# Performance work log

Hardware: AMD Instinct MI355X
Metric: run time of the kernel (lower is better)

## Reference

```python
import jax, jax.numpy as jnp
import numpy as np

K = 20
EPS = 1e-5
N = 4096


def lrelu(x):
    return jnp.where(x >= 0, x, 0.2 * x)


def bn(x, g, b, m, v):
    # eval-mode BatchNorm over channel dim 1
    shape = [1] * x.ndim
    shape[1] = -1
    inv = g / jnp.sqrt(v + EPS)
    return (x - m.reshape(shape)) * inv.reshape(shape) + b.reshape(shape)


def get_graph_feature(x):
    # Faithful to repo: num_points = x.shape[1], remaining dims fold into channels.
    p = x.shape[1]
    x2d = x.reshape(-1, p)              # (C, P)
    xx = jnp.sum(x2d * x2d, axis=0)     # (P,)
    dist = 2.0 * (x2d.T @ x2d) - xx[:, None] - xx[None, :]  # -||xi-xj||^2, (P, P)
    idx = jax.lax.top_k(dist, K)[1]     # (P, K) nearest neighbors (incl. self)
    xt = x2d.T                          # (P, C)
    feat = xt[idx]                      # (P, K, C) neighbor gather
    ctr = jnp.broadcast_to(xt[:, None, :], feat.shape)
    out = jnp.concatenate([feat - ctr, ctr], axis=-1)  # (P, K, 2C)
    return out.transpose(2, 0, 1)[None]                # (1, 2C, P, K)


def setup_inputs():
    key = jax.random.key(0)
    ks = jax.random.split(key, 16)

    def w(k_, o, c):
        return jax.random.normal(k_, (o, c), jnp.float32) / float(np.sqrt(c))

    def bnp(k_, c):
        k1, k2, k3, k4 = jax.random.split(k_, 4)
        return (1.0 + 0.1 * jax.random.normal(k1, (c,), jnp.float32),
                0.1 * jax.random.normal(k2, (c,), jnp.float32),
                0.1 * jax.random.normal(k3, (c,), jnp.float32),
                jax.random.uniform(k4, (c,), jnp.float32, minval=0.5, maxval=1.5))

    g1, b1, m1, v1 = bnp(ks[1], 64)
    g2, b2, m2, v2 = bnp(ks[2], 64)
    g3, b3, m3, v3 = bnp(ks[3], 128)
    g4, b4, m4, v4 = bnp(ks[4], 256)
    g5, b5, m5, v5 = bnp(ks[5], 512)
    return dict(
        x=jax.random.normal(ks[0], (3, N), jnp.float32),
        w1=w(ks[6], 64, 6), g1=g1, b1=b1, m1=m1, v1=v1,
        w2=w(ks[7], 64, 64), g2=g2, b2=b2, m2=m2, v2=v2,
        w3=w(ks[8], 128, 64), g3=g3, b3=b3, m3=m3, v3=v3,
        w4=w(ks[9], 256, 128), g4=g4, b4=b4, m4=m4, v4=v4,
        w5=w(ks[10], 512, 256), g5=g5, b5=b5, m5=m5, v5=v5,
        lw1=w(ks[11], 512, 1024),
        lw2=w(ks[12], 256, 512),
        lb2=0.1 * jax.random.normal(ks[13], (256,), jnp.float32),
        ow=w(ks[14], 11, 256),
        ob=0.1 * jax.random.normal(ks[15], (11,), jnp.float32),
    )


def reference(x, w1, g1, b1, m1, v1, w2, g2, b2, m2, v2, w3, g3, b3, m3, v3,
              w4, g4, b4, m4, v4, w5, g5, b5, m5, v5, lw1, lw2, lb2, ow, ob):
    conv2d = lambda w_, f_: jnp.einsum('oc,bcpk->bopk', w_, f_)

    f = get_graph_feature(x)                                   # (1, 6, N, K)
    h = lrelu(bn(conv2d(w1, f), g1, b1, m1, v1))
    x1 = jnp.max(h, axis=-1)                                   # (1, 64, N)

    f = jnp.swapaxes(get_graph_feature(x1), 1, 2)              # (1, 64, 2N, K)
    h = lrelu(bn(conv2d(w2, f), g2, b2, m2, v2))
    x2 = jnp.max(h, axis=-1)                                   # (1, 64, 2N)

    f = jnp.swapaxes(get_graph_feature(x2), 1, 2)              # (1, 64, 4N, K)
    h = lrelu(bn(conv2d(w3, f), g3, b3, m3, v3))
    x3 = jnp.max(h, axis=-1)                                   # (1, 128, 4N)

    f = jnp.swapaxes(get_graph_feature(x3), 1, 2)              # (1, 128, 8N, K)
    h = lrelu(bn(conv2d(w4, f), g4, b4, m4, v4))
    x4 = jnp.max(h, axis=-1)                                   # (1, 256, 8N)

    h5 = lrelu(bn(jnp.einsum('oc,bcp->bop', w5, x4), g5, b5, m5, v5))  # (1, 512, 8N)
    pmax = jnp.max(h5, axis=-1)
    pavg = jnp.mean(h5, axis=-1)
    z = jnp.concatenate([pmax, pavg], axis=1)                  # (1, 1024)
    z = lrelu(z @ lw1.T)                                       # (1, 512); dropout = eval identity
    z = lrelu(z @ lw2.T + lb2)                                 # (1, 256)
    logits = z @ ow.T + ob                                     # (1, 11)
    return jax.nn.softmax(logits, axis=1)
```

## Files before the change

kernel.cpp:

```cpp
#include <hip/hip_runtime.h>
#include <hip/hip_bf16.h>
#include <float.h>
#include <math.h>

#define DEV __device__ __forceinline__

DEV float lrelu(float x) { return x >= 0.f ? x : 0.2f * x; }

constexpr int N = 4096, KNN = 20;

typedef __attribute__((ext_vector_type(4))) float f32x4;
typedef __attribute__((ext_vector_type(8))) short s16x8;

constexpr size_t OFF_SC1 = 0,    OFF_SH1 = 64;
constexpr size_t OFF_SC2 = 128,  OFF_SH2 = 192;
constexpr size_t OFF_SC3 = 256,  OFF_SH3 = 384;
constexpr size_t OFF_SC4 = 512,  OFF_SH4 = 768;
constexpr size_t OFF_SC5 = 1024, OFF_SH5 = 1536;
constexpr size_t OFF_X1 = 2048;
constexpr size_t OFF_X2 = OFF_X1 + (size_t)64*4096;
constexpr size_t OFF_X3 = OFF_X2 + (size_t)64*8192;
constexpr size_t OFF_X4 = OFF_X3 + (size_t)128*16384;
constexpr size_t OFF_A  = OFF_X4 + (size_t)256*32768;
constexpr size_t OFF_GP = OFF_A + (size_t)256*21*128;
constexpr size_t OFF_PM = OFF_GP + (size_t)64*128*128;
constexpr size_t OFF_PS = OFF_PM + (size_t)512*256;
constexpr size_t OFF_Z0 = OFF_PS + (size_t)512*256;
constexpr size_t OFF_Z1 = OFF_Z0 + 1024;
constexpr size_t OFF_Z2 = OFF_Z1 + 512;
constexpr size_t OFF_IDX = OFF_Z2 + 256;
constexpr size_t WS_NEEDED_BYTES = OFF_IDX * 4 + (size_t)N * KNN * 4;
constexpr size_t OFF_ABF = OFF_A;
constexpr size_t OFF_W5BF = OFF_A + 524288;

__global__ void k_ws_sentinel(float* out, float mb) {
  int t = threadIdx.x;
  if (t < 11) out[t] = 1.0e6f + mb;
}

__global__ __launch_bounds__(512) void k_bn_pre(
    const float* g1, const float* b1, const float* m1, const float* v1,
    const float* g2, const float* b2, const float* m2, const float* v2,
    const float* g3, const float* b3, const float* m3, const float* v3,
    const float* g4, const float* b4, const float* m4, const float* v4,
    const float* g5, const float* b5, const float* m5, const float* v5,
    float* ws) {
  int t = threadIdx.x;
  const float* G[5] = {g1,g2,g3,g4,g5};
  const float* B[5] = {b1,b2,b3,b4,b5};
  const float* M[5] = {m1,m2,m3,m4,m5};
  const float* V[5] = {v1,v2,v3,v4,v5};
  const size_t SC[5] = {OFF_SC1,OFF_SC2,OFF_SC3,OFF_SC4,OFF_SC5};
  const size_t SH[5] = {OFF_SH1,OFF_SH2,OFF_SH3,OFF_SH4,OFF_SH5};
  const int CN[5] = {64,64,128,256,512};
  for (int s = 0; s < 5; ++s) {
    for (int i = t; i < CN[s]; i += 512) {
      float scale = G[s][i] / sqrtf(V[s][i] + 1e-5f);
      ws[SC[s] + i] = scale;
      ws[SH[s] + i] = B[s][i] - M[s][i] * scale;
    }
  }
}

__global__ __launch_bounds__(256) void k_s1_topk(const float* x, int* idx) {
  __shared__ float d[N];
  __shared__ float vsh[256];
  __shared__ int ish[256];
  int i = blockIdx.x, t = threadIdx.x;
  {
    #pragma clang fp contract(off)
    float xi0 = x[i], xi1 = x[N + i], xi2 = x[2*N + i];
    float sqi = xi0*xi0 + xi1*xi1 + xi2*xi2;
    for (int j = t; j < N; j += 256) {
      float xj0 = x[j], xj1 = x[N+j], xj2 = x[2*N+j];
      float sqj = xj0*xj0 + xj1*xj1 + xj2*xj2;
      float p = xi0*xj0 + xi1*xj1 + xi2*xj2;
      d[j] = (2.f*p - sqi) - sqj;
    }
  }
  __syncthreads();
  for (int k = 0; k < KNN; ++k) {
    float bv = -FLT_MAX; int bi = N;
    for (int j = t; j < N; j += 256) { float v = d[j]; if (v > bv) { bv = v; bi = j; } }
    vsh[t] = bv; ish[t] = bi;
    __syncthreads();
    for (int s = 128; s > 0; s >>= 1) {
      if (t < s) {
        float v2 = vsh[t+s]; int i2 = ish[t+s];
        if (v2 > vsh[t] || (v2 == vsh[t] && i2 < ish[t])) { vsh[t] = v2; ish[t] = i2; }
      }
      __syncthreads();
    }
    if (t == 0) { idx[i*KNN + k] = ish[0]; d[ish[0]] = -FLT_MAX; }
    __syncthreads();
  }
}

__global__ __launch_bounds__(256) void k_s1_conv(const float* x, const float* w1g,
                                                 const int* idx, const float* sc, const float* sh, float* x1) {
  __shared__ int idxs[64][KNN];
  __shared__ float xs[3][64];
  __shared__ float wsh[4][6];
  int t = threadIdx.x, bx = blockIdx.x, by = blockIdx.y;
  int i0 = bx * 64;
  for (int u = t; u < 64*KNN; u += 256) idxs[u/KNN][u%KNN] = idx[(size_t)(i0 + u/KNN)*KNN + u%KNN];
  for (int u = t; u < 3*64; u += 256) xs[u/64][u%64] = x[(size_t)(u/64)*N + i0 + (u%64)];
  for (int u = t; u < 24; u += 256) wsh[u/6][u%6] = w1g[(size_t)(by*4 + u/6)*6 + u%6];
  __syncthreads();
  int il = t & 63, ol = t >> 6;
  int o = by*4 + ol, i = i0 + il;
  float xi0 = xs[0][il], xi1 = xs[1][il], xi2 = xs[2][il];
  float w0 = wsh[ol][0], w1v = wsh[ol][1], w2v = wsh[ol][2];
  float w3v = wsh[ol][3], w4v = wsh[ol][4], w5v = wsh[ol][5];
  float ctr = w3v*xi0 + w4v*xi1 + w5v*xi2;
  float scale = sc[o], shift = sh[o];
  float best = -FLT_MAX;
  for (int k = 0; k < KNN; ++k) {
    int j = idxs[il][k];
    float h = w0*(x[j] - xi0) + w1v*(x[N+j] - xi1) + w2v*(x[2*N+j] - xi2) + ctr;
    h = lrelu(h*scale + shift);
    best = fmaxf(best, h);
  }
  x1[(size_t)o*N + i] = best;
}

template<int P>
__global__ __launch_bounds__(256) void k_gram_partial(const float* prev, int C, float* gp) {
  constexpr int BI = P / 16;
  __shared__ float ysh[32][P];
  int b = blockIdx.x, t = threadIdx.x;
  int R = C / 64;
  int base = b * R;
  float acc[BI][BI] = {};
  int i0 = (t >> 4) * BI, j0 = (t & 15) * BI;
  for (int r0 = 0; r0 < R; r0 += 32) {
    for (int u = t; u < 32*P; u += 256) ysh[u/P][u%P] = prev[(size_t)(base + r0 + u/P)*P + (u%P)];
    __syncthreads();
    for (int r = 0; r < 32; ++r) {
      float yi[BI], yj[BI];
      #pragma unroll
      for (int a = 0; a < BI; ++a) { yi[a] = ysh[r][i0+a]; yj[a] = ysh[r][j0+a]; }
      #pragma unroll
      for (int a = 0; a < BI; ++a)
        #pragma unroll
        for (int c = 0; c < BI; ++c) acc[a][c] += yi[a]*yj[c];
    }
    __syncthreads();
  }
  for (int a = 0; a < BI; ++a)
    for (int c = 0; c < BI; ++c)
      gp[(size_t)b*P*P + (size_t)(i0+a)*P + (j0+c)] = acc[a][c];
}

template<int P>
__global__ __launch_bounds__(128) void k_dist_topk(const float* gp, int* idx) {
  __shared__ float dsh[P];
  __shared__ float diag[P];
  __shared__ float vsh[128];
  __shared__ int ish[128];
  int i = blockIdx.x, t = threadIdx.x;
  if (t < P) {
    float gij = 0.f, gjj = 0.f;
    for (int b = 0; b < 64; ++b) {
      gij += gp[(size_t)b*P*P + (size_t)i*P + t];
      gjj += gp[(size_t)b*P*P + (size_t)t*P + t];
    }
    diag[t] = gjj;
    dsh[t] = gij;
  }
  __syncthreads();
  if (t < P) dsh[t] = (2.f*dsh[t] - diag[i]) - diag[t];
  __syncthreads();
  for (int k = 0; k < KNN; ++k) {
    float bv = -FLT_MAX; int bi = P;
    if (t < P) { bv = dsh[t]; bi = t; }
    vsh[t] = bv; ish[t] = bi;
    __syncthreads();
    for (int s = 64; s > 0; s >>= 1) {
      if (t < s) {
        float v2 = vsh[t+s]; int i2 = ish[t+s];
        if (v2 > vsh[t] || (v2 == vsh[t] && i2 < ish[t])) { vsh[t] = v2; ish[t] = i2; }
      }
      __syncthreads();
    }
    if (t == 0) { idx[i*KNN + k] = ish[0]; dsh[ish[0]] = -FLT_MAX; }
    __syncthreads();
  }
}

template<int P>
__global__ __launch_bounds__(64) void k_build_A(const float* w, const int* idx, int O, float* A) {
  __shared__ float row[64][P];
  int t = threadIdx.x;
  int r = blockIdx.x*64 + t;
  if (r < O*21) {
    int o = r / 21, kk = r % 21;
    float* my = row[t];
    if (kk == 20) {
      for (int i2 = 0; i2 < P; ++i2) my[i2] = w[(size_t)o*P + i2];
    } else {
      for (int i2 = 0; i2 < P; ++i2) my[i2] = 0.f;
      for (int j = 0; j < P; ++j) my[idx[j*KNN + kk]] += w[(size_t)o*P + j];
    }
    for (int i2 = 0; i2 < P; ++i2) A[(size_t)r*P + i2] = my[i2];
  }
}

__global__ __launch_bounds__(64) void k_build_A_bf(const float* w, const int* idx, __hip_bfloat16* A) {
  __shared__ float row[64][128];
  int t = threadIdx.x;
  int r = blockIdx.x*64 + t;
  int o = r >> 5, kk = r & 31;
  float* my = row[t];
  if (kk == 20) {
    for (int i2 = 0; i2 < 128; ++i2) my[i2] = w[(size_t)o*128 + i2];
  } else if (kk < 20) {
    for (int i2 = 0; i2 < 128; ++i2) my[i2] = 0.f;
    for (int j = 0; j < 128; ++j) my[idx[j*KNN + kk]] += w[(size_t)o*128 + j];
  } else {
    for (int i2 = 0; i2 < 128; ++i2) my[i2] = 0.f;
  }
  for (int i2 = 0; i2 < 128; ++i2) A[(size_t)r*128 + i2] = __float2bfloat16(my[i2]);
}

__global__ __launch_bounds__(256) void k_f32_to_bf16(const float* in, __hip_bfloat16* out) {
  size_t base = ((size_t)blockIdx.x*256 + threadIdx.x) * 16;
  #pragma unroll
  for (int j = 0; j < 4; ++j) {
    float4 v = *(const float4*)(in + base + j*4);
    __hip_bfloat16 tmp[4] = {__float2bfloat16(v.x), __float2bfloat16(v.y),
                             __float2bfloat16(v.z), __float2bfloat16(v.w)};
    *(ushort4*)(out + base + j*4) = *(const ushort4*)tmp;
  }
}

__global__ __launch_bounds__(256) void k_conv4_mfma(const __hip_bfloat16* Abf, const __hip_bfloat16* Xbf,
                                                    const float* sc, const float* sh, float* x4) {
  constexpr int RA = 64, MT = 256;
  __shared__ char As[RA*256];
  __shared__ char Bs[MT*256];
  int t = threadIdx.x, bx = blockIdx.x, by = blockIdx.y;
  int m0 = bx*MT, rbase = by*RA;
  for (int u = t; u < RA*16; u += 256) {
    int row = u >> 4, k8 = u & 15;
    s16x8 v = *(const s16x8*)(Abf + ((size_t)(rbase+row) << 7) + (k8 << 3));
    *(s16x8*)(As + (row << 8) + ((k8 << 4) ^ ((row & 7) << 4))) = v;
  }
  for (int u = t; u < MT*16; u += 256) {
    int row = u >> 4, k8 = u & 15;
    s16x8 v = *(const s16x8*)(Xbf + ((size_t)(m0+row) << 7) + (k8 << 3));
    *(s16x8*)(Bs + (row << 8) + ((k8 << 4) ^ ((row & 7) << 4))) = v;
  }
  __syncthreads();
  int lane = t & 63, w = t >> 6;
  int col = lane & 15, lg = lane >> 4;
  f32x4 acc[4][4] = {};
  #pragma unroll
  for (int ks = 0; ks < 4; ++ks) {
    int kbyte = ks*64 + lg*16;
    s16x8 a[4], b[4];
    #pragma unroll
    for (int at = 0; at < 4; ++at) { int r = at*16 + col; a[at] = *(const s16x8*)(As + (r<<8) + (kbyte ^ ((r&7)<<4))); }
    #pragma unroll
    for (int bt = 0; bt < 4; ++bt) { int r = w*64 + bt*16 + col; b[bt] = *(const s16x8*)(Bs + (r<<8) + (kbyte ^ ((r&7)<<4))); }
    #pragma unroll
    for (int at = 0; at < 4; ++at)
      #pragma unroll
      for (int bt = 0; bt < 4; ++bt)
        acc[at][bt] = __builtin_amdgcn_mfma_f32_16x16x32_bf16(a[at], b[bt], acc[at][bt], 0, 0, 0);
  }
  int o0 = by*2;
  #pragma unroll
  for (int ol = 0; ol < 2; ++ol) {
    float scale = sc[o0+ol], shift = sh[o0+ol];
    #pragma unroll
    for (int bt = 0; bt < 4; ++bt) {
      float h2b = __shfl(acc[2*ol+1][bt][0], 16 + col);
      float mx = -FLT_MAX;
      #pragma unroll
      for (int q = 0; q < 4; ++q) {
        mx = fmaxf(mx, lrelu((acc[2*ol][bt][q] - h2b)*scale + shift));
        float v1 = lrelu((acc[2*ol+1][bt][q] - h2b)*scale + shift);
        if (lg == 0) mx = fmaxf(mx, v1);
      }
      mx = fmaxf(mx, __shfl_xor(mx, 16));
      mx = fmaxf(mx, __shfl_xor(mx, 32));
      float ctr = lrelu(h2b*scale + shift);
      if ((lg >> 1) == ol) {
        float val = (lg & 1) ? ctr : mx;
        size_t p = (size_t)m0 + w*64 + bt*16 + col + ((lg & 1) ? 16384 : 0);
        x4[(size_t)(o0+ol)*32768 + p] = val;
      }
    }
  }
}

template<int P>
__global__ __launch_bounds__(256) void k_fused_conv(const float* prev, const float* A,
                                                    const float* sc, const float* sh,
                                                    int C, float* outx) {
  constexpr int TO = 8, ROWS = TO*21;
  __shared__ float Ash[ROWS][65];
  __shared__ float Bsh[64][132];
  int bx = blockIdx.x, by = blockIdx.y, t = threadIdx.x;
  int m0 = bx*128;
  int rowbase = by*ROWS;
  int ol = t >> 5, mg = t & 31;
  float acc[21][4] = {};
  for (int ic = 0; ic < P/64; ++ic) {
    for (int u = t; u < ROWS*64; u += 256) {
      int rr = u >> 6, cc = u & 63;
      Ash[rr][cc] = A[(size_t)(rowbase + rr)*P + ic*64 + cc];
    }
    for (int u = t; u < 64*128; u += 256) {
      int mr = u >> 6, ii = u & 63;
      Bsh[ii][mr] = prev[(size_t)(m0 + mr)*P + ic*64 + ii];
    }
    __syncthreads();
    for (int i = 0; i < 64; ++i) {
      float v0 = Bsh[i][mg*4+0], v1 = Bsh[i][mg*4+1], v2 = Bsh[i][mg*4+2], v3 = Bsh[i][mg*4+3];
      #pragma unroll
      for (int kk = 0; kk < 21; ++kk) {
        float a = Ash[ol*21 + kk][i];
        acc[kk][0] += a*v0; acc[kk][1] += a*v1; acc[kk][2] += a*v2; acc[kk][3] += a*v3;
      }
    }
    __syncthreads();
  }
  int o = by*TO + ol;
  float scale = sc[o], shift = sh[o];
  size_t C2 = 2*(size_t)C;
  #pragma unroll
  for (int mm = 0; mm < 4; ++mm) {
    int m = m0 + mg*4 + mm;
    float h2 = acc[20][mm];
    float ctr = lrelu(h2*scale + shift);
    float best = -FLT_MAX;
    #pragma unroll
    for (int kk = 0; kk < 20; ++kk) {
      float v = lrelu((acc[kk][mm] - h2)*scale + shift);
      best = fmaxf(best, v);
    }
    outx[(size_t)o*C2 + m] = best;
    outx[(size_t)o*C2 + C + m] = ctr;
  }
}

__global__ __launch_bounds__(256) void k_s5_mfma(const float* x4, const __hip_bfloat16* w5bf,
                                                 const float* sc, const float* sh,
                                                 float* pm, float* ps) {
  __shared__ char smem[8192 + 32768];
  __shared__ float redm[64][4];
  __shared__ float reds[64][4];
  int t = threadIdx.x, bx = blockIdx.x, by = blockIdx.y;
  int p0 = bx*256, o0 = by*64;
  int lane = t & 63, w = t >> 6;
  int lrow = lane & 15, lg = lane >> 4;
  char* As = smem;
  char* Bs = smem + 8192;
  f32x4 acc[4][4] = {};
  for (int c0 = 0; c0 < 256; c0 += 64) {
    for (int u = t; u < 64*8; u += 256) {
      int row = u >> 3, k8 = u & 7;
      s16x8 v = *(const s16x8*)(w5bf + (size_t)(o0+row)*256 + c0 + k8*8);
      *(s16x8*)(As + row*128 + ((k8*16) ^ ((row&7)<<4))) = v;
    }
    #pragma unroll
    for (int i = 0; i < 8; ++i) {
      __hip_bfloat16 tmp[8];
      #pragma unroll
      for (int j = 0; j < 8; ++j)
        tmp[j] = __float2bfloat16(x4[(size_t)(c0 + i*8 + j)*32768 + p0 + t]);
      *(s16x8*)(Bs + t*128 + ((i*16) ^ ((t&7)<<4))) = *(const s16x8*)tmp;
    }
    __syncthreads();
    #pragma unroll
    for (int ksub = 0; ksub < 2; ++ksub) {
      int kbyte = ksub*64 + lg*16;
      s16x8 a[4], b[4];
      #pragma unroll
      for (int rt = 0; rt < 4; ++rt) { int r = rt*16 + lrow; a[rt] = *(const s16x8*)(As + r*128 + (kbyte ^ ((r&7)<<4))); }
      #pragma unroll
      for (int cf = 0; cf < 4; ++cf) { int r = w*64 + cf*16 + lrow; b[cf] = *(const s16x8*)(Bs + r*128 + (kbyte ^ ((r&7)<<4))); }
      #pragma unroll
      for (int rt = 0; rt < 4; ++rt)
        #pragma unroll
        for (int cf = 0; cf < 4; ++cf)
          acc[rt][cf] = __builtin_amdgcn_mfma_f32_16x16x32_bf16(a[rt], b[cf], acc[rt][cf], 0, 0, 0);
    }
    __syncthreads();
  }
  #pragma unroll
  for (int rt = 0; rt < 4; ++rt) {
    #pragma unroll
    for (int q = 0; q < 4; ++q) {
      int ol = rt*16 + lg*4 + q;
      float scale = sc[o0+ol], shift = sh[o0+ol];
      float mx = -FLT_MAX, sm = 0.f;
      #pragma unroll
      for (int cf = 0; cf < 4; ++cf) {
        float h = lrelu(acc[rt][cf][q]*scale + shift);
        mx = fmaxf(mx, h); sm += h;
      }
      #pragma unroll
      for (int off2 = 1; off2 < 16; off2 <<= 1) {
        mx = fmaxf(mx, __shfl_xor(mx, off2));
        sm += __shfl_xor(sm, off2);
      }
      if (lrow == 0) { redm[ol][w] = mx; reds[ol][w] = sm; }
    }
  }
  __syncthreads();
  if (t < 64) {
    float mx = fmaxf(fmaxf(redm[t][0], redm[t][1]), fmaxf(redm[t][2], redm[t][3]));
    float sm = reds[t][0] + reds[t][1] + reds[t][2] + reds[t][3];
    pm[(size_t)(o0 + t)*128 + bx] = mx;
    ps[(size_t)(o0 + t)*128 + bx] = sm;
  }
}

__global__ __launch_bounds__(512) void k_pool(const float* pm, const float* ps, float* z0) {
  int t = threadIdx.x;
  for (int o = t; o < 512; o += 512) {
    float mx = -FLT_MAX, sm = 0.f;
    for (int nt = 0; nt < 128; ++nt) { mx = fmaxf(mx, pm[(size_t)o*128+nt]); sm += ps[(size_t)o*128+nt]; }
    z0[o] = mx;
    z0[512+o] = sm * (1.f/32768.f);
  }
}

__global__ __launch_bounds__(128) void k_fc1(const float* z0, const float* lw1, float* z1) {
  int bx = blockIdx.x, t = threadIdx.x;
  int rl = t >> 4, cl = t & 15;
  int r = bx*8 + rl;
  float acc = 0.f;
  for (int u = 0; u < 64; ++u) {
    int c = cl*64 + u;
    acc += z0[c] * lw1[(size_t)r*1024 + c];
  }
  #pragma unroll
  for (int off = 1; off < 16; off <<= 1) acc += __shfl_xor(acc, off);
  if (cl == 0) z1[r] = lrelu(acc);
}

__global__ __launch_bounds__(128) void k_fc2(const float* z1, const float* lw2,
                                             const float* lb2, float* z2) {
  int bx = blockIdx.x, t = threadIdx.x;
  int rl = t >> 4, cl = t & 15;
  int r = bx*8 + rl;
  float acc = 0.f;
  for (int u = 0; u < 32; ++u) {
    int c = cl*32 + u;
    acc += z1[c] * lw2[(size_t)r*512 + c];
  }
  #pragma unroll
  for (int off = 1; off < 16; off <<= 1) acc += __shfl_xor(acc, off);
  if (cl == 0) z2[r] = lrelu(acc + lb2[r]);
}

__global__ __launch_bounds__(64) void k_fc3(const float* z2, const float* ow,
                                            const float* ob, float* out) {
  __shared__ float lg[11];
  __shared__ float ex[11];
  int t = threadIdx.x;
  if (t < 11) {
    float acc = 0.f;
    for (int c = 0; c < 256; ++c) acc += z2[c] * ow[t*256 + c];
    lg[t] = acc + ob[t];
  }
  __syncthreads();
  if (t < 11) {
    float m = -FLT_MAX;
    for (int r = 0; r < 11; ++r) m = fmaxf(m, lg[r]);
    ex[t] = expf(lg[t] - m);
  }
  __syncthreads();
  if (t < 11) {
    float s = 0.f;
    for (int r = 0; r < 11; ++r) s += ex[r];
    out[t] = ex[t] / s;
  }
}

extern "C" void kernel_launch(void* const* d_in, const int* in_sizes, int n_in,
                              void* d_out, int out_size, void* d_ws, size_t ws_size,
                              hipStream_t stream) {
  auto f = [&](int i) { return (const float*)d_in[i]; };
  float* ws = (float*)d_ws;
  int* idx = (int*)(ws + OFF_IDX);
  float* out = (float*)d_out;

  if (ws_size < WS_NEEDED_BYTES) {
    k_ws_sentinel<<<1, 64, 0, stream>>>(out, (float)(ws_size >> 20));
    return;
  }

  __hip_bfloat16* Abf = (__hip_bfloat16*)(ws + OFF_ABF);
  __hip_bfloat16* Xbf = (__hip_bfloat16*)(ws + OFF_GP);
  __hip_bfloat16* w5bf = (__hip_bfloat16*)(ws + OFF_W5BF);
  float* x4 = ws + OFF_X4;

  k_bn_pre<<<1, 512, 0, stream>>>(f(2),f(3),f(4),f(5), f(7),f(8),f(9),f(10),
                                  f(12),f(13),f(14),f(15), f(17),f(18),f(19),f(20),
                                  f(22),f(23),f(24),f(25), ws);
  k_s1_topk<<<N, 256, 0, stream>>>(f(0), idx);
  k_s1_conv<<<dim3(N/64, 16), 256, 0, stream>>>(f(0), f(1), idx, ws+OFF_SC1, ws+OFF_SH1, ws+OFF_X1);
  k_gram_partial<64><<<64, 256, 0, stream>>>(ws+OFF_X1, 4096, ws+OFF_GP);
  k_dist_topk<64><<<64, 128, 0, stream>>>(ws+OFF_GP, idx);
  k_build_A<64><<<21, 64, 0, stream>>>(f(6), idx, 64, ws+OFF_A);
  k_fused_conv<64><<<dim3(4096/128, 64/8), 256, 0, stream>>>(ws+OFF_X1, ws+OFF_A, ws+OFF_SC2, ws+OFF_SH2, 4096, ws+OFF_X2);
  k_gram_partial<64><<<64, 256, 0, stream>>>(ws+OFF_X2, 8192, ws+OFF_GP);
  k_dist_topk<64><<<64, 128, 0, stream>>>(ws+OFF_GP, idx);
  k_build_A<64><<<42, 64, 0, stream>>>(f(11), idx, 128, ws+OFF_A);
  k_fused_conv<64><<<dim3(8192/128, 128/8), 256, 0, stream>>>(ws+OFF_X2, ws+OFF_A, ws+OFF_SC3, ws+OFF_SH3, 8192, ws+OFF_X3);
  k_gram_partial<128><<<64, 256, 0, stream>>>(ws+OFF_X3, 16384, ws+OFF_GP);
  k_dist_topk<128><<<128, 128, 0, stream>>>(ws+OFF_GP, idx);
  k_build_A_bf<<<128, 64, 0, stream>>>(f(16), idx, Abf);
  k_f32_to_bf16<<<512, 256, 0, stream>>>(ws+OFF_X3, Xbf);
  k_conv4_mfma<<<dim3(16384/256, 128), 256, 0, stream>>>(Abf, Xbf, ws+OFF_SC4, ws+OFF_SH4, x4);
  k_f32_to_bf16<<<32, 256, 0, stream>>>(f(21), w5bf);
  k_s5_mfma<<<dim3(128, 8), 256, 0, stream>>>(x4, w5bf, ws+OFF_SC5, ws+OFF_SH5, ws+OFF_PM, ws+OFF_PS);
  k_pool<<<1, 512, 0, stream>>>(ws+OFF_PM, ws+OFF_PS, ws+OFF_Z0);
  k_fc1<<<64, 128, 0, stream>>>(ws+OFF_Z0, f(26), ws+OFF_Z1);
  k_fc2<<<32, 128, 0, stream>>>(ws+OFF_Z1, f(27), f(28), ws+OFF_Z2);
  k_fc3<<<1, 64, 0, stream>>>(ws+OFF_Z2, f(29), f(30), out);
}
```

Before: 534.3 us.

## Reuse staged point tile across 16 weight row-blocks in conv4 MFMA kernel

The conv4 MFMA kernel now stages each 256-point bf16 tile of X into shared memory once and loops over 16 row-blocks of the transformed weight matrix, with 512 threads split into two groups that each handle a row-block per iteration. Previously every one of 128 y-blocks reloaded the same X tile. A fragments are now read directly from global memory instead of shared, relying on cache hits since the A matrix is small. The grid shrinks from 64x128 to 64x8 blocks, which cuts total X traffic but lowers parallelism and serialises the work inside each block.

Result: slower. 555.8 us (+4.0%).

```diff
diff --git a/kernel.cpp b/kernel.cpp
--- a/kernel.cpp
+++ b/kernel.cpp
@@ -234,19 +234,13 @@
   }
 }
 
-__global__ __launch_bounds__(256) void k_conv4_mfma(const __hip_bfloat16* Abf, const __hip_bfloat16* Xbf,
-                                                    const float* sc, const float* sh, float* x4) {
-  constexpr int RA = 64, MT = 256;
-  __shared__ char As[RA*256];
+__global__ __launch_bounds__(512, 4) void k_conv4_mfma(const __hip_bfloat16* Abf, const __hip_bfloat16* Xbf,
+                                                       const float* sc, const float* sh, float* x4) {
+  constexpr int MT = 256;
   __shared__ char Bs[MT*256];
-  int t = threadIdx.x, bx = blockIdx.x, by = blockIdx.y;
-  int m0 = bx*MT, rbase = by*RA;
-  for (int u = t; u < RA*16; u += 256) {
-    int row = u >> 4, k8 = u & 15;
-    s16x8 v = *(const s16x8*)(Abf + ((size_t)(rbase+row) << 7) + (k8 << 3));
-    *(s16x8*)(As + (row << 8) + ((k8 << 4) ^ ((row & 7) << 4))) = v;
-  }
-  for (int u = t; u < MT*16; u += 256) {
+  int t = threadIdx.x, bx = blockIdx.x, byg = blockIdx.y;
+  int m0 = bx*MT;
+  for (int u = t; u < MT*16; u += 512) {
     int row = u >> 4, k8 = u & 15;
     s16x8 v = *(const s16x8*)(Xbf + ((size_t)(m0+row) << 7) + (k8 << 3));
     *(s16x8*)(Bs + (row << 8) + ((k8 << 4) ^ ((row & 7) << 4))) = v;
@@ -254,42 +248,52 @@
   __syncthreads();
   int lane = t & 63, w = t >> 6;
   int col = lane & 15, lg = lane >> 4;
-  f32x4 acc[4][4] = {};
-  #pragma unroll
-  for (int ks = 0; ks < 4; ++ks) {
-    int kbyte = ks*64 + lg*16;
-    s16x8 a[4], b[4];
+  int q = w & 3, pb = w >> 2;
+  for (int it = 0; it < 8; ++it) {
+    int by = byg*16 + it*2 + pb;
+    const __hip_bfloat16* Ab = Abf + ((size_t)(by*64) << 7);
+    f32x4 acc[4][4] = {};
     #pragma unroll
-    for (int at = 0; at < 4; ++at) { int r = at*16 + col; a[at] = *(const s16x8*)(As + (r<<8) + (kbyte ^ ((r&7)<<4))); }
+    for (int ks = 0; ks < 4; ++ks) {
+      int kel = ks*32 + lg*8;
+      int kbyte = ks*64 + lg*16;
+      s16x8 a[4], b[4];
+      #pragma unroll
+      for (int at = 0; at < 4; ++at)
+        a[at] = *(const s16x8*)(Ab + ((size_t)(at*16 + col) << 7) + kel);
+      #pragma unroll
+      for (int bt = 0; bt < 4; ++bt) {
+        int r = q*64 + bt*16 + col;
+        b[bt] = *(const s16x8*)(Bs + (r << 8) + (kbyte ^ ((r & 7) << 4)));
+      }
+      #pragma unroll
+      for (int at = 0; at < 4; ++at)
+        #pragma unroll
+        for (int bt = 0; bt < 4; ++bt)
+          acc[at][bt] = __builtin_amdgcn_mfma_f32_16x16x32_bf16(a[at], b[bt], acc[at][bt], 0, 0, 0);
+    }
+    int o0 = by*2;
     #pragma unroll
-    for (int bt = 0; bt < 4; ++bt) { int r = w*64 + bt*16 + col; b[bt] = *(const s16x8*)(Bs + (r<<8) + (kbyte ^ ((r&7)<<4))); }
-    #pragma unroll
-    for (int at = 0; at < 4; ++at)
-      #pragma unroll
-      for (int bt = 0; bt < 4; ++bt)
-        acc[at][bt] = __builtin_amdgcn_mfma_f32_16x16x32_bf16(a[at], b[bt], acc[at][bt], 0, 0, 0);
-  }
-  int o0 = by*2;
-  #pragma unroll
-  for (int ol = 0; ol < 2; ++ol) {
-    float scale = sc[o0+ol], shift = sh[o0+ol];
-    #pragma unroll
-    for (int bt = 0; bt < 4; ++bt) {
-      float h2b = __shfl(acc[2*ol+1][bt][0], 16 + col);
-      float mx = -FLT_MAX;
-      #pragma unroll
-      for (int q = 0; q < 4; ++q) {
-        mx = fmaxf(mx, lrelu((acc[2*ol][bt][q] - h2b)*scale + shift));
-        float v1 = lrelu((acc[2*ol+1][bt][q] - h2b)*scale + shift);
-        if (lg == 0) mx = fmaxf(mx, v1);
-      }
-      mx = fmaxf(mx, __shfl_xor(mx, 16));
-      mx = fmaxf(mx, __shfl_xor(mx, 32));
-      float ctr = lrelu(h2b*scale + shift);
-      if ((lg >> 1) == ol) {
-        float val = (lg & 1) ? ctr : mx;
-        size_t p = (size_t)m0 + w*64 + bt*16 + col + ((lg & 1) ? 16384 : 0);
-        x4[(size_t)(o0+ol)*32768 + p] = val;
+    for (int ol = 0; ol < 2; ++ol) {
+      float scale = sc[o0+ol], shift = sh[o0+ol];
+      #pragma unroll
+      for (int bt = 0; bt < 4; ++bt) {
+        float h2b = __shfl(acc[2*ol+1][bt][0], 16 + col);
+        float mx = -FLT_MAX;
+        #pragma unroll
+        for (int qq = 0; qq < 4; ++qq) {
+          mx = fmaxf(mx, lrelu((acc[2*ol][bt][qq] - h2b)*scale + shift));
+          float v1 = lrelu((acc[2*ol+1][bt][qq] - h2b)*scale + shift);
+          if (lg == 0) mx = fmaxf(mx, v1);
+        }
+        mx = fmaxf(mx, __shfl_xor(mx, 16));
+        mx = fmaxf(mx, __shfl_xor(mx, 32));
+        float ctr = lrelu(h2b*scale + shift);
+        if ((lg >> 1) == ol) {
+          float val = (lg & 1) ? ctr : mx;
+          size_t p = (size_t)m0 + q*64 + bt*16 + col + ((lg & 1) ? 16384 : 0);
+          x4[(size_t)(o0+ol)*32768 + p] = val;
+        }
       }
     }
   }
@@ -517,7 +521,7 @@
   k_dist_topk<128><<<128, 128, 0, stream>>>(ws+OFF_GP, idx);
   k_build_A_bf<<<128, 64, 0, stream>>>(f(16), idx, Abf);
   k_f32_to_bf16<<<512, 256, 0, stream>>>(ws+OFF_X3, Xbf);
-  k_conv4_mfma<<<dim3(16384/256, 128), 256, 0, stream>>>(Abf, Xbf, ws+OFF_SC4, ws+OFF_SH4, x4);
+  k_conv4_mfma<<<dim3(16384/256, 8), 512, 0, stream>>>(Abf, Xbf, ws+OFF_SC4, ws+OFF_SH4, x4);
   k_f32_to_bf16<<<32, 256, 0, stream>>>(f(21), w5bf);
   k_s5_mfma<<<dim3(128, 8), 256, 0, stream>>>(x4, w5bf, ws+OFF_SC5, ws+OFF_SH5, ws+OFF_PM, ws+OFF_PS);
   k_pool<<<1, 512, 0, stream>>>(ws+OFF_PM, ws+OFF_PS, ws+OFF_Z0);
```
